# Optimization experiments

Hardware: AMD Instinct MI355X
Metric: run time of the kernel (lower is better)

The kernel has to match this reference:

```python
import jax, jax.numpy as jnp
import numpy as np

SAMPLE_RATE = 16000
SOUND_SPEED = 343.0
MAX_ORDER = 15
RIR_LENGTH = 3968
WINDOW_LENGTH = 81
PAD = WINDOW_LENGTH // 2  # 40

# Static image-source lattice (depends only on max_order): all integer
# reflection index triplets with |nx|+|ny|+|nz| <= max_order.
_ind = np.arange(-MAX_ORDER, MAX_ORDER + 1)
_grid = np.stack(np.meshgrid(_ind, _ind, _ind, indexing="ij"), -1).reshape(-1, 3)
XYZ = _grid[np.abs(_grid).sum(1) <= MAX_ORDER].astype(np.float32)  # (I,3), I=4991
EXP_LO = np.abs(np.floor(XYZ / 2)).astype(np.float32)        # hits on lower walls per dim
EXP_HI = np.abs(np.floor((XYZ + 1) / 2)).astype(np.float32)  # hits on upper walls per dim


def _hann(x, T):
    # continuous Hann window sampled at non-integer points, zero outside |x|<=T/2
    return jnp.where(jnp.abs(x) <= T / 2, 0.5 * (1.0 + jnp.cos(2.0 * jnp.pi * x / T)), 0.0)


def _forward(inp):
    room = inp[:, 0:3]                 # (B,3) room dimensions [m]
    mic = inp[:, 3:6] * room           # (B,3)
    src = inp[:, 6:9] * room           # (B,3)
    a_w = inp[:, 9:10]
    absorption = jnp.concatenate([a_w, a_w, a_w, a_w, inp[:, 10:11], inp[:, 11:12]], axis=1)
    absorption = absorption * 0.84 + 0.01            # (B,6): [x-,x+,y-,y+,floor,ceiling]
    tr = jnp.sqrt(1.0 - absorption)                  # wall reflection coefficients

    xyz = jnp.asarray(XYZ)                           # (I,3)
    d = room[:, None, :]
    s = src[:, None, :]
    # image source locations (B,I,3): mirror parity per torchaudio ISM
    img_loc = jnp.where(xyz % 2 == 1, d * (xyz + 1.0) - s, d * xyz + s)
    # per-image-source attenuation (B,I)
    t_lo = tr[:, None, 0::2]                         # (B,1,3) lower walls per dim
    t_hi = tr[:, None, 1::2]                         # (B,1,3) upper walls per dim
    att = jnp.prod(t_lo ** jnp.asarray(EXP_LO) * t_hi ** jnp.asarray(EXP_HI), axis=-1)

    dist = jnp.linalg.norm(img_loc - mic[:, None, :], axis=-1)   # (B,I)
    amp = att / dist                                              # 1/r spreading
    delay = dist * (SAMPLE_RATE / SOUND_SPEED)                    # fractional sample delay
    delay_i = jnp.ceil(delay)

    # windowed-sinc fractional-delay pulse sampled at n = delay_i-PAD .. delay_i+PAD
    n_rel = jnp.arange(-PAD, PAD + 1, dtype=jnp.float32)          # (W,)
    x = delay_i[..., None] + n_rel - delay[..., None]             # (B,I,W)
    sig = amp[..., None] * jnp.sinc(x) * _hann(x, 2 * PAD)        # (B,I,W)

    # scatter-accumulate pulses at time index n, dropping out-of-range samples
    t_idx = (delay_i[..., None] + n_rel).astype(jnp.int32)        # (B,I,W)
    B = inp.shape[0]
    b_idx = jnp.arange(B, dtype=jnp.int32)[:, None, None]
    rir = jnp.zeros((B, RIR_LENGTH), dtype=sig.dtype).at[b_idx, t_idx].add(sig, mode="drop")

    toa = PAD + SAMPLE_RATE * jnp.linalg.norm(mic - src, axis=1) / SOUND_SPEED  # (B,)
    return rir, toa


def setup_inputs():
    key = jax.random.key(0)
    u = jax.random.uniform(key, (128, 12), dtype=jnp.float32)
    room = 2.0 + 8.0 * u[:, :3]          # room dims in [2,10] m
    rest = 0.05 + 0.9 * u[:, 3:]         # mic/src fractions and absorptions in (0,1)
    return {"input": jnp.concatenate([room, rest], axis=1)}


def reference(input):
    return _forward(input)
```

## Files before the change

kernel.cpp:

```cpp
#include <hip/hip_runtime.h>

#define NIMG    4991
#define RIRLEN  3968
#define NT      512
#define NTP     1024
#define NTG     256
#define NGRPF   16
#define GGRP    32
#define CAP     2048
#define CAPG    1024
#define KPT     10
#define KPTP    5
#define INV_PI  0.31830988618379067f
#define SR_OVER_C 46.647230320699704f

struct Tab { int v[NIMG]; };
static constexpr Tab make_tab() {
    Tab t{};
    int k = 0;
    for (int x = -15; x <= 15; ++x)
        for (int y = -15; y <= 15; ++y)
            for (int z = -15; z <= 15; ++z) {
                int ax = x < 0 ? -x : x;
                int ay = y < 0 ? -y : y;
                int az = z < 0 ? -z : z;
                if (ax + ay + az <= 15)
                    t.v[k++] = (x + 15) | ((y + 15) << 8) | ((z + 15) << 16);
            }
    return t;
}
__constant__ Tab c_tab = make_tab();

static __device__ __forceinline__ int iabs(int v) { return v < 0 ? -v : v; }
static __device__ __forceinline__ int imin(int a, int b) { return a < b ? a : b; }
static __device__ __forceinline__ int imax(int a, int b) { return a > b ? a : b; }

typedef __fp16 f16x2 __attribute__((ext_vector_type(2)));


__global__ __launch_bounds__(NTP)
void rir_prep(const float* __restrict__ inp, float* __restrict__ out,
              float2* __restrict__ wdh, unsigned* __restrict__ wcs,
              int* __restrict__ offs, int B) {
    const int b    = blockIdx.x;
    const int tid  = threadIdx.x;
    const int lane = tid & 63;
    const int wv   = tid >> 6;
    const int q    = lane & 3;

    __shared__ float s_par[12];
    __shared__ float s_p2[3][32];
    __shared__ float s_at[3][32];
    __shared__ int   s_h4[256][4];
    __shared__ int   s_off[257];

    if (tid < 1024) ((int*)s_h4)[tid] = 0;
    if (tid == 0) {
        const float* ip = inp + b * 12;
        float rx = ip[0], ry = ip[1], rz = ip[2];
        float mx = ip[3] * rx, my = ip[4] * ry, mz = ip[5] * rz;
        float sx = ip[6] * rx, sy = ip[7] * ry, sz = ip[8] * rz;
        float aw = __builtin_fmaf(ip[9],  0.84f, 0.01f);
        float a4 = __builtin_fmaf(ip[10], 0.84f, 0.01f);
        float a5 = __builtin_fmaf(ip[11], 0.84f, 0.01f);
        s_par[0] = rx; s_par[1] = ry; s_par[2] = rz;
        s_par[3] = mx; s_par[4] = my; s_par[5] = mz;
        s_par[6] = sx; s_par[7] = sy; s_par[8] = sz;
        s_par[9]  = 0.5f * __builtin_amdgcn_logf(1.0f - aw);
        s_par[10] = 0.5f * __builtin_amdgcn_logf(1.0f - a4);
        s_par[11] = 0.5f * __builtin_amdgcn_logf(1.0f - a5);
        float dx = mx - sx, dy = my - sy, dz = mz - sz;
        out[(size_t)B * RIRLEN + b] = __builtin_fmaf(
            __builtin_sqrtf(dx * dx + dy * dy + dz * dz), SR_OVER_C, 40.0f);
    }
    __syncthreads();

    if (tid < 96) {
        const int axis = tid >> 5;
        const int j    = tid & 31;
        if (j < 31) {
            const int n = j - 15;
            const float rr = s_par[axis];
            const float mm = s_par[3 + axis];
            const float ss = s_par[6 + axis];
            const float iv = (n & 1) ? __builtin_fmaf(rr, (float)(n + 1), -ss)
                                     : __builtin_fmaf(rr, (float)n, ss);
            const float pv = iv - mm;
            s_p2[axis][j] = pv * pv;
            const float e4 = (float)iabs(n >> 1);
            const float e5 = (float)iabs((n + 1) >> 1);
            const float ex = (axis < 2)
                ? (e4 + e5) * s_par[9]
                : __builtin_fmaf(e4, s_par[10], e5 * s_par[11]);
            s_at[axis][j] = __builtin_amdgcn_exp2f(ex);
        }
    }
    __syncthreads();

    float2   edh[KPTP];
    unsigned ecs[KPTP];
    int      enc[KPTP];
    #pragma unroll
    for (int k = 0; k < KPTP; ++k) {
        enc[k] = -1;
        const int idx = tid + k * NTP;
        if (idx < NIMG) {
            const int p  = c_tab.v[idx];
            const int xi = p & 255;
            const int yi = (p >> 8) & 255;
            const int zi = (p >> 16) & 255;
            const float d2   = s_p2[0][xi] + s_p2[1][yi] + s_p2[2][zi];
            const float dist = __builtin_sqrtf(d2);
            const float delay = dist * SR_OVER_C;
            const float di    = __builtin_ceilf(delay);
            const int   ti0   = (int)di - 40;
            if (ti0 < RIRLEN) {
                const int bk = (ti0 + 96) >> 4;
                const float att = s_at[0][xi] * s_at[1][yi] * s_at[2][zi];
                const float amp = att * __builtin_amdgcn_rcpf(dist);
                float frac = di - delay;
                if (frac == 0.0f) frac = di * 1.52587890625e-05f;
                const int dii = (int)di;
                float c1p = amp * __builtin_amdgcn_sinf(0.5f * frac) * INV_PI;
                if (dii & 1) c1p = -c1p;
                const float Hp     = 0.5f * c1p;
                const float dstore = di - frac;
                const float rv = dstore * 0.0125f;
                const float fr = rv - __builtin_floorf(rv);
                const float Hcd = Hp * __builtin_amdgcn_cosf(fr);
                const float Hsd = Hp * __builtin_amdgcn_sinf(fr);
                const f16x2 pk2 = __builtin_amdgcn_cvt_pkrtz(Hcd, Hsd);

                const int rnk = atomicAdd(&s_h4[bk][q], 1);
                enc[k] = (bk << 13) | rnk;
                edh[k] = make_float2(dstore, Hp);
                ecs[k] = __builtin_bit_cast(unsigned, pk2);
            }
        }
    }
    __syncthreads();

    if (wv == 0) {
        const int l = lane;
        const int4 a0 = *(const int4*)&s_h4[4 * l + 0][0];
        const int4 a1 = *(const int4*)&s_h4[4 * l + 1][0];
        const int4 a2 = *(const int4*)&s_h4[4 * l + 2][0];
        const int4 a3 = *(const int4*)&s_h4[4 * l + 3][0];
        const int c0 = a0.x + a0.y + a0.z + a0.w;
        const int c1 = a1.x + a1.y + a1.z + a1.w;
        const int c2 = a2.x + a2.y + a2.z + a2.w;
        const int c3 = a3.x + a3.y + a3.z + a3.w;
        const int ts = c0 + c1 + c2 + c3;
        int incl = ts;
        #pragma unroll
        for (int d = 1; d < 64; d <<= 1) {
            const int u = __shfl_up(incl, d, 64);
            if (l >= d) incl += u;
        }
        const int base = incl - ts;
        s_off[4 * l + 0] = base;
        s_off[4 * l + 1] = base + c0;
        s_off[4 * l + 2] = base + c0 + c1;
        s_off[4 * l + 3] = base + c0 + c1 + c2;
        if (l == 63) s_off[256] = incl;
    }
    __syncthreads();

    if (tid < 256) {
        int run = s_off[tid];
        #pragma unroll
        for (int p = 0; p < 4; ++p) {
            const int c = s_h4[tid][p];
            s_h4[tid][p] = run;
            run += c;
        }
    }
    __syncthreads();

    float2*   db = wdh + (size_t)b * NIMG;
    unsigned* cb = wcs + (size_t)b * NIMG;
    #pragma unroll
    for (int k = 0; k < KPTP; ++k) {
        if (enc[k] >= 0) {
            const int bk   = enc[k] >> 13;
            const int slot = s_h4[bk][q] + (enc[k] & 8191);
            db[slot] = edh[k];
            cb[slot] = ecs[k];
        }
    }
    if (tid < 257) offs[b * 257 + tid] = s_off[tid];
}

__global__ __launch_bounds__(NTG, 8)
void rir_gather(const float2* __restrict__ wdh, const unsigned* __restrict__ wcs,
                const int* __restrict__ offs, float* __restrict__ out, int B) {
    const int bx   = blockIdx.x;
    const int b    = bx >> 5;
    const int g    = bx & 31;
    const int tid  = threadIdx.x;
    const int lane = tid & 63;
    const int wv   = tid >> 6;

    __shared__ __align__(16) float2   s_dh[CAPG];
    __shared__ __align__(16) unsigned s_cs[CAPG];
    __shared__ float s_acc[2][64];

    if (tid < 128) ((float*)s_acc)[tid] = 0.0f;

    const int* ob = offs + b * 257;
    int wlo[2], wlen[2], wpre[2];
    int T = 0, nw = 0;
    #pragma unroll
    for (int kk = 0; kk < 2; ++kk) {
        const int wi = g + 32 * kk;
        wpre[kk] = T;
        if (wi < 62) {
            wlo[kk] = ob[4 * wi + 1];
            int len = ob[4 * wi + 10] - wlo[kk];
            if (T + len > CAPG) len = CAPG - T;
            if (len < 0) len = 0;
            wlen[kk] = len;
            T += len;
            nw = kk + 1;
        } else { wlo[kk] = 0; wlen[kk] = 0; }
    }

    const float2*   db = wdh + (size_t)b * NIMG;
    const unsigned* cb = wcs + (size_t)b * NIMG;
    for (int j = tid; j < T; j += NTG) {
        const int kk  = (j >= wpre[1] && wlen[1] > 0) ? 1 : 0;
        const int src = wlo[kk] + (j - wpre[kk]);
        s_dh[j] = db[src];
        s_cs[j] = cb[src];
    }
    __syncthreads();

    const int a0r = (T * wv) >> 2;
    const int a1r = (T * (wv + 1)) >> 2;

#define EV1(ACC, DLY, HPV, PKU) do {                                         \
        const f16x2 hh = __builtin_bit_cast(f16x2, (PKU));                   \
        const float xw = tf - (DLY);                                         \
        const float pre = __builtin_fmaf(cth0, (float)hh.x,                  \
                              __builtin_fmaf(sth0, (float)hh.y, (HPV)));     \
        const float hm = (__builtin_fabsf(xw) <= 40.0f) ? pre : 0.0f;        \
        ACC = __builtin_fmaf(hm, __builtin_amdgcn_rcpf(xw), ACC);            \
    } while (0)

    #pragma unroll
    for (int kk = 0; kk < 2; ++kk) {
        if (wlen[kk] == 0) continue;
        int       i  = imax(wpre[kk], a0r);
        const int ie = imin(wpre[kk] + wlen[kk], a1r);
        if (i >= ie) continue;

        const int   wi   = g + 32 * kk;
        const int   t    = (wi << 6) + lane;
        const float tf   = (float)t;
        const int   m    = t - (t / 80) * 80;
        const float cth0 = __builtin_amdgcn_cosf((float)m * 0.0125f);
        const float sth0 = __builtin_amdgcn_sinf((float)m * 0.0125f);

        float acc0 = 0.0f, acc1 = 0.0f;
        while (i < ie && (i & 3)) { EV1(acc0, s_dh[i].x, s_dh[i].y, s_cs[i]); ++i; }
        for (; i + 4 <= ie; i += 4) {
            const float4 d0 = *(const float4*)&s_dh[i];
            const float4 d1 = *(const float4*)&s_dh[i + 2];
            const uint4  cc = *(const uint4*)&s_cs[i];
            EV1(acc0, d0.x, d0.y, cc.x); EV1(acc1, d0.z, d0.w, cc.y);
            EV1(acc0, d1.x, d1.y, cc.z); EV1(acc1, d1.z, d1.w, cc.w);
        }
        for (; i < ie; ++i) EV1(acc0, s_dh[i].x, s_dh[i].y, s_cs[i]);

        atomicAdd(&s_acc[kk][lane], acc0 + acc1);
    }
#undef EV1
    __syncthreads();

    if (tid < 64 * nw) {
        const int kk = tid >> 6;
        const int wi = g + 32 * kk;
        const int t  = (wi << 6) + lane;
        const float sl = (lane & 1) ? -1.0f : 1.0f;
        out[(size_t)b * RIRLEN + t] = sl * s_acc[kk][lane];
    }
}

__global__ __launch_bounds__(NT, 8)
void rir_fused(const float* __restrict__ inp, float* __restrict__ out, int B) {
    const int bx   = blockIdx.x;
    const int b    = bx >> 4;
    const int g    = bx & 15;
    const int tid  = threadIdx.x;
    const int lane = tid & 63;
    const int wv   = tid >> 6;
    const int q    = lane & 3;

    __shared__ __align__(16) float2   s_dh[CAP];
    __shared__ __align__(16) unsigned s_cs[CAP];
    __shared__ float    s_par[12];
    __shared__ float    s_p2[3][32];
    __shared__ float    s_at[3][32];
    __shared__ int      s_h4[256][4];
    __shared__ int      s_off[257];
    __shared__ float    s_acc[4][64];

    for (int k = tid; k < 1024; k += NT) ((int*)s_h4)[k] = 0;
    if (tid < 256) ((float*)s_acc)[tid] = 0.0f;
    if (tid == 0) {
        const float* ip = inp + b * 12;
        float rx = ip[0], ry = ip[1], rz = ip[2];
        float mx = ip[3] * rx, my = ip[4] * ry, mz = ip[5] * rz;
        float sx = ip[6] * rx, sy = ip[7] * ry, sz = ip[8] * rz;
        float aw = __builtin_fmaf(ip[9],  0.84f, 0.01f);
        float a4 = __builtin_fmaf(ip[10], 0.84f, 0.01f);
        float a5 = __builtin_fmaf(ip[11], 0.84f, 0.01f);
        s_par[0] = rx; s_par[1] = ry; s_par[2] = rz;
        s_par[3] = mx; s_par[4] = my; s_par[5] = mz;
        s_par[6] = sx; s_par[7] = sy; s_par[8] = sz;
        s_par[9]  = 0.5f * __builtin_amdgcn_logf(1.0f - aw);
        s_par[10] = 0.5f * __builtin_amdgcn_logf(1.0f - a4);
        s_par[11] = 0.5f * __builtin_amdgcn_logf(1.0f - a5);
        if (g == 0) {
            float dx = mx - sx, dy = my - sy, dz = mz - sz;
            out[(size_t)B * RIRLEN + b] = __builtin_fmaf(
                __builtin_sqrtf(dx * dx + dy * dy + dz * dz), SR_OVER_C, 40.0f);
        }
    }
    __syncthreads();

    if (tid < 96) {
        const int axis = tid >> 5;
        const int j    = tid & 31;
        if (j < 31) {
            const int n = j - 15;
            const float rr = s_par[axis];
            const float mm = s_par[3 + axis];
            const float ss = s_par[6 + axis];
            const float iv = (n & 1) ? __builtin_fmaf(rr, (float)(n + 1), -ss)
                                     : __builtin_fmaf(rr, (float)n, ss);
            const float pv = iv - mm;
            s_p2[axis][j] = pv * pv;
            const float e4 = (float)iabs(n >> 1);
            const float e5 = (float)iabs((n + 1) >> 1);
            const float ex = (axis < 2)
                ? (e4 + e5) * s_par[9]
                : __builtin_fmaf(e4, s_par[10], e5 * s_par[11]);
            s_at[axis][j] = __builtin_amdgcn_exp2f(ex);
        }
    }
    __syncthreads();

    const int fb = 4 * g + 1;

    float2   edh[KPT];
    unsigned ecs[KPT];
    int      enc[KPT];
    #pragma unroll
    for (int k = 0; k < KPT; ++k) {
        enc[k] = -1;
        const int idx = tid + k * NT;
        if (idx < NIMG) {
            const int p  = c_tab.v[idx];
            const int xi = p & 255;
            const int yi = (p >> 8) & 255;
            const int zi = (p >> 16) & 255;
            const float d2   = s_p2[0][xi] + s_p2[1][yi] + s_p2[2][zi];
            const float dist = __builtin_sqrtf(d2);
            const float delay = dist * SR_OVER_C;
            const float di    = __builtin_ceilf(delay);
            const int   ti0   = (int)di - 40;
            const int   bk    = (ti0 + 96) >> 4;
            const bool owned  = ((unsigned)((bk - fb + 64) & 63) < 9u);
            if (ti0 < RIRLEN && owned) {
                const float att = s_at[0][xi] * s_at[1][yi] * s_at[2][zi];
                const float amp = att * __builtin_amdgcn_rcpf(dist);
                float frac = di - delay;
                if (frac == 0.0f) frac = di * 1.52587890625e-05f;
                const int dii = (int)di;
                float c1p = amp * __builtin_amdgcn_sinf(0.5f * frac) * INV_PI;
                if (dii & 1) c1p = -c1p;
                const float Hp     = 0.5f * c1p;
                const float dstore = di - frac;
                const float rv = dstore * 0.0125f;
                const float fr = rv - __builtin_floorf(rv);
                const float Hcd = Hp * __builtin_amdgcn_cosf(fr);
                const float Hsd = Hp * __builtin_amdgcn_sinf(fr);
                const f16x2 pk2 = __builtin_amdgcn_cvt_pkrtz(Hcd, Hsd);
                const int rnk = atomicAdd(&s_h4[bk][q], 1);
                enc[k] = (bk << 13) | rnk;
                edh[k] = make_float2(dstore, Hp);
                ecs[k] = __builtin_bit_cast(unsigned, pk2);
            }
        }
    }
    __syncthreads();

    if (wv == 0) {
        const int l = lane;
        const int4 a0 = *(const int4*)&s_h4[4 * l + 0][0];
        const int4 a1 = *(const int4*)&s_h4[4 * l + 1][0];
        const int4 a2 = *(const int4*)&s_h4[4 * l + 2][0];
        const int4 a3 = *(const int4*)&s_h4[4 * l + 3][0];
        const int c0 = a0.x + a0.y + a0.z + a0.w;
        const int c1 = a1.x + a1.y + a1.z + a1.w;
        const int c2 = a2.x + a2.y + a2.z + a2.w;
        const int c3 = a3.x + a3.y + a3.z + a3.w;
        const int ts = c0 + c1 + c2 + c3;
        int incl = ts;
        #pragma unroll
        for (int d = 1; d < 64; d <<= 1) {
            const int u = __shfl_up(incl, d, 64);
            if (l >= d) incl += u;
        }
        const int base = incl - ts;
        s_off[4 * l + 0] = imin(base, CAP);
        s_off[4 * l + 1] = imin(base + c0, CAP);
        s_off[4 * l + 2] = imin(base + c0 + c1, CAP);
        s_off[4 * l + 3] = imin(base + c0 + c1 + c2, CAP);
        if (l == 63) s_off[256] = imin(incl, CAP);
    }
    __syncthreads();

    if (tid < 256) {
        int run = s_off[tid];
        #pragma unroll
        for (int p = 0; p < 4; ++p) {
            const int c = s_h4[tid][p];
            s_h4[tid][p] = run;
            run += c;
        }
    }
    __syncthreads();

    #pragma unroll
    for (int k = 0; k < KPT; ++k) {
        if (enc[k] >= 0) {
            const int bk   = enc[k] >> 13;
            const int slot = s_h4[bk][q] + (enc[k] & 8191);
            if (slot < CAP) {
                s_dh[slot] = edh[k];
                s_cs[slot] = ecs[k];
            }
        }
    }
    __syncthreads();

    int wlo[4], wlen[4], wpre[4];
    int T = 0, nw = 0;
    #pragma unroll
    for (int kk = 0; kk < 4; ++kk) {
        const int wi = g + 16 * kk;
        wpre[kk] = T;
        if (wi < 62) {
            wlo[kk]  = s_off[4 * wi + 1];
            wlen[kk] = s_off[4 * wi + 10] - wlo[kk];
            T += wlen[kk];
            nw = kk + 1;
        } else { wlo[kk] = 0; wlen[kk] = 0; }
    }
    const int a0r = (T * wv) >> 3;
    const int a1r = (T * (wv + 1)) >> 3;

#define EV1(ACC, DLY, HPV, PKU) do {                                         \
        const f16x2 hh = __builtin_bit_cast(f16x2, (PKU));                   \
        const float xw = tf - (DLY);                                         \
        const float pre = __builtin_fmaf(cth0, (float)hh.x,                  \
                              __builtin_fmaf(sth0, (float)hh.y, (HPV)));     \
        const float hm = (__builtin_fabsf(xw) <= 40.0f) ? pre : 0.0f;        \
        ACC = __builtin_fmaf(hm, __builtin_amdgcn_rcpf(xw), ACC);            \
    } while (0)

    #pragma unroll
    for (int kk = 0; kk < 4; ++kk) {
        if (wlen[kk] == 0) continue;
        const int o0 = imax(wpre[kk], a0r);
        const int oe = imin(wpre[kk] + wlen[kk], a1r);
        if (o0 >= oe) continue;
        int       i  = wlo[kk] + (o0 - wpre[kk]);
        const int ie = wlo[kk] + (oe - wpre[kk]);

        const int   wi   = g + 16 * kk;
        const int   t    = (wi << 6) + lane;
        const float tf   = (float)t;
        const int   m    = t - (t / 80) * 80;
        const float cth0 = __builtin_amdgcn_cosf((float)m * 0.0125f);
        const float sth0 = __builtin_amdgcn_sinf((float)m * 0.0125f);

        float acc0 = 0.0f, acc1 = 0.0f;
        while (i < ie && (i & 3)) { EV1(acc0, s_dh[i].x, s_dh[i].y, s_cs[i]); ++i; }
        for (; i + 4 <= ie; i += 4) {
            const float4 d0 = *(const float4*)&s_dh[i];
            const float4 d1 = *(const float4*)&s_dh[i + 2];
            const uint4  cc = *(const uint4*)&s_cs[i];
            EV1(acc0, d0.x, d0.y, cc.x); EV1(acc1, d0.z, d0.w, cc.y);
            EV1(acc0, d1.x, d1.y, cc.z); EV1(acc1, d1.z, d1.w, cc.w);
        }
        for (; i < ie; ++i) EV1(acc0, s_dh[i].x, s_dh[i].y, s_cs[i]);

        atomicAdd(&s_acc[kk][lane], acc0 + acc1);
    }
#undef EV1
    __syncthreads();

    if (tid < 64 * nw) {
        const int kk = tid >> 6;
        const int wi = g + 16 * kk;
        const int t  = (wi << 6) + lane;
        const float sl = (lane & 1) ? -1.0f : 1.0f;
        out[(size_t)b * RIRLEN + t] = sl * s_acc[kk][lane];
    }
}

extern "C" void kernel_launch(void* const* d_in, const int* in_sizes, int n_in,
                              void* d_out, int out_size, void* d_ws, size_t ws_size,
                              hipStream_t stream) {
    (void)n_in; (void)out_size;
    const float* inp = (const float*)d_in[0];
    float* out = (float*)d_out;
    const int B = in_sizes[0] / 12;

    const size_t dh_bytes   = (size_t)B * NIMG * sizeof(float2);
    const size_t cs_bytes   = (size_t)B * NIMG * sizeof(unsigned);
    const size_t offs_bytes = (size_t)B * 257 * sizeof(int);
    const int use_ws = (d_ws != nullptr &&
                        ws_size >= dh_bytes + cs_bytes + offs_bytes) ? 1 : 0;

    if (use_ws) {
        float2*   wdh  = (float2*)d_ws;
        unsigned* wcs  = (unsigned*)((char*)d_ws + dh_bytes);
        int*      offs = (int*)((char*)d_ws + dh_bytes + cs_bytes);
        rir_prep  <<<dim3(B),        dim3(NTP), 0, stream>>>(inp, out, wdh, wcs, offs, B);
        rir_gather<<<dim3(B * GGRP), dim3(NTG), 0, stream>>>(wdh, wcs, offs, out, B);
    } else {
        rir_fused<<<dim3(B * NGRPF), dim3(NT), 0, stream>>>(inp, out, B);
    }
}
```

Before: 104.9 us.

## Pack pulse records as float4 and pair mirrored windows in gather blocks

Prep now writes each image-source record as a single float4 (delay, Hp, Hcd, Hsd) in fp32 instead of a float2 plus a packed fp16 pair. Gather stages one float4 array in LDS and reads it with simpler per-element vector loads. Each gather block now handles windows g and 61-g rather than g and g+32, which balances early dense and late sparse windows across 31 blocks per batch, and the LDS capacity is raised to match. The price is more global and LDS traffic per record and a larger LDS footprint, which may reduce occupancy.

```diff
diff --git a/kernel.cpp b/kernel.cpp
--- a/kernel.cpp
+++ b/kernel.cpp
@@ -6,9 +6,9 @@
 #define NTP     1024
 #define NTG     256
 #define NGRPF   16
-#define GGRP    32
+#define GGRP    31
 #define CAP     2048
-#define CAPG    1024
+#define CAPG    1152
 #define KPT     10
 #define KPTP    5
 #define INV_PI  0.31830988618379067f
@@ -40,8 +40,7 @@
 
 __global__ __launch_bounds__(NTP)
 void rir_prep(const float* __restrict__ inp, float* __restrict__ out,
-              float2* __restrict__ wdh, unsigned* __restrict__ wcs,
-              int* __restrict__ offs, int B) {
+              float4* __restrict__ wq, int* __restrict__ offs, int B) {
     const int b    = blockIdx.x;
     const int tid  = threadIdx.x;
     const int lane = tid & 63;
@@ -97,9 +96,8 @@
     }
     __syncthreads();
 
-    float2   edh[KPTP];
-    unsigned ecs[KPTP];
-    int      enc[KPTP];
+    float4 ef[KPTP];
+    int    enc[KPTP];
     #pragma unroll
     for (int k = 0; k < KPTP; ++k) {
         enc[k] = -1;
@@ -129,12 +127,10 @@
                 const float fr = rv - __builtin_floorf(rv);
                 const float Hcd = Hp * __builtin_amdgcn_cosf(fr);
                 const float Hsd = Hp * __builtin_amdgcn_sinf(fr);
-                const f16x2 pk2 = __builtin_amdgcn_cvt_pkrtz(Hcd, Hsd);
 
                 const int rnk = atomicAdd(&s_h4[bk][q], 1);
                 enc[k] = (bk << 13) | rnk;
-                edh[k] = make_float2(dstore, Hp);
-                ecs[k] = __builtin_bit_cast(unsigned, pk2);
+                ef[k]  = make_float4(dstore, Hp, Hcd, Hsd);
             }
         }
     }
@@ -177,73 +173,64 @@
     }
     __syncthreads();
 
-    float2*   db = wdh + (size_t)b * NIMG;
-    unsigned* cb = wcs + (size_t)b * NIMG;
+    float4* qb = wq + (size_t)b * NIMG;
     #pragma unroll
     for (int k = 0; k < KPTP; ++k) {
         if (enc[k] >= 0) {
             const int bk   = enc[k] >> 13;
             const int slot = s_h4[bk][q] + (enc[k] & 8191);
-            db[slot] = edh[k];
-            cb[slot] = ecs[k];
+            qb[slot] = ef[k];
         }
     }
     if (tid < 257) offs[b * 257 + tid] = s_off[tid];
 }
 
 __global__ __launch_bounds__(NTG, 8)
-void rir_gather(const float2* __restrict__ wdh, const unsigned* __restrict__ wcs,
-                const int* __restrict__ offs, float* __restrict__ out, int B) {
+void rir_gather(const float4* __restrict__ wq, const int* __restrict__ offs,
+                float* __restrict__ out, int B) {
     const int bx   = blockIdx.x;
-    const int b    = bx >> 5;
-    const int g    = bx & 31;
+    const int b    = bx / GGRP;
+    const int g    = bx - b * GGRP;
     const int tid  = threadIdx.x;
     const int lane = tid & 63;
     const int wv   = tid >> 6;
 
-    __shared__ __align__(16) float2   s_dh[CAPG];
-    __shared__ __align__(16) unsigned s_cs[CAPG];
+    __shared__ __align__(16) float4 s_e[CAPG];
     __shared__ float s_acc[2][64];
 
     if (tid < 128) ((float*)s_acc)[tid] = 0.0f;
 
+    const int wis[2] = { g, 61 - g };
     const int* ob = offs + b * 257;
     int wlo[2], wlen[2], wpre[2];
-    int T = 0, nw = 0;
+    int T = 0;
     #pragma unroll
     for (int kk = 0; kk < 2; ++kk) {
-        const int wi = g + 32 * kk;
+        const int wi = wis[kk];
         wpre[kk] = T;
-        if (wi < 62) {
-            wlo[kk] = ob[4 * wi + 1];
-            int len = ob[4 * wi + 10] - wlo[kk];
-            if (T + len > CAPG) len = CAPG - T;
-            if (len < 0) len = 0;
-            wlen[kk] = len;
-            T += len;
-            nw = kk + 1;
-        } else { wlo[kk] = 0; wlen[kk] = 0; }
-    }
-
-    const float2*   db = wdh + (size_t)b * NIMG;
-    const unsigned* cb = wcs + (size_t)b * NIMG;
+        wlo[kk]  = ob[4 * wi + 1];
+        int len  = ob[4 * wi + 10] - wlo[kk];
+        if (T + len > CAPG) len = CAPG - T;
+        if (len < 0) len = 0;
+        wlen[kk] = len;
+        T += len;
+    }
+
+    const float4* qb = wq + (size_t)b * NIMG;
     for (int j = tid; j < T; j += NTG) {
         const int kk  = (j >= wpre[1] && wlen[1] > 0) ? 1 : 0;
-        const int src = wlo[kk] + (j - wpre[kk]);
-        s_dh[j] = db[src];
-        s_cs[j] = cb[src];
+        s_e[j] = qb[wlo[kk] + (j - wpre[kk])];
     }
     __syncthreads();
 
     const int a0r = (T * wv) >> 2;
     const int a1r = (T * (wv + 1)) >> 2;
 
-#define EV1(ACC, DLY, HPV, PKU) do {                                         \
-        const f16x2 hh = __builtin_bit_cast(f16x2, (PKU));                   \
-        const float xw = tf - (DLY);                                         \
-        const float pre = __builtin_fmaf(cth0, (float)hh.x,                  \
-                              __builtin_fmaf(sth0, (float)hh.y, (HPV)));     \
-        const float hm = (__builtin_fabsf(xw) <= 40.0f) ? pre : 0.0f;        \
+#define EV1(ACC, E) do {                                                     \
+        const float xw  = tf - (E).x;                                        \
+        const float pre = __builtin_fmaf(cth0, (E).z,                        \
+                              __builtin_fmaf(sth0, (E).w, (E).y));           \
+        const float hm  = (__builtin_fabsf(xw) <= 40.0f) ? pre : 0.0f;       \
         ACC = __builtin_fmaf(hm, __builtin_amdgcn_rcpf(xw), ACC);            \
     } while (0)
 
@@ -254,7 +241,7 @@
         const int ie = imin(wpre[kk] + wlen[kk], a1r);
         if (i >= ie) continue;
 
-        const int   wi   = g + 32 * kk;
+        const int   wi   = wis[kk];
         const int   t    = (wi << 6) + lane;
         const float tf   = (float)t;
         const int   m    = t - (t / 80) * 80;
@@ -262,24 +249,21 @@
         const float sth0 = __builtin_amdgcn_sinf((float)m * 0.0125f);
 
         float acc0 = 0.0f, acc1 = 0.0f;
-        while (i < ie && (i & 3)) { EV1(acc0, s_dh[i].x, s_dh[i].y, s_cs[i]); ++i; }
         for (; i + 4 <= ie; i += 4) {
-            const float4 d0 = *(const float4*)&s_dh[i];
-            const float4 d1 = *(const float4*)&s_dh[i + 2];
-            const uint4  cc = *(const uint4*)&s_cs[i];
-            EV1(acc0, d0.x, d0.y, cc.x); EV1(acc1, d0.z, d0.w, cc.y);
-            EV1(acc0, d1.x, d1.y, cc.z); EV1(acc1, d1.z, d1.w, cc.w);
-        }
-        for (; i < ie; ++i) EV1(acc0, s_dh[i].x, s_dh[i].y, s_cs[i]);
+            const float4 e0 = s_e[i],     e1 = s_e[i + 1];
+            const float4 e2 = s_e[i + 2], e3 = s_e[i + 3];
+            EV1(acc0, e0); EV1(acc1, e1); EV1(acc0, e2); EV1(acc1, e3);
+        }
+        for (; i < ie; ++i) { const float4 e = s_e[i]; EV1(acc0, e); }
 
         atomicAdd(&s_acc[kk][lane], acc0 + acc1);
     }
 #undef EV1
     __syncthreads();
 
-    if (tid < 64 * nw) {
+    if (tid < 128) {
         const int kk = tid >> 6;
-        const int wi = g + 32 * kk;
+        const int wi = wis[kk];
         const int t  = (wi << 6) + lane;
         const float sl = (lane & 1) ? -1.0f : 1.0f;
         out[(size_t)b * RIRLEN + t] = sl * s_acc[kk][lane];
@@ -520,18 +504,15 @@
     float* out = (float*)d_out;
     const int B = in_sizes[0] / 12;
 
-    const size_t dh_bytes   = (size_t)B * NIMG * sizeof(float2);
-    const size_t cs_bytes   = (size_t)B * NIMG * sizeof(unsigned);
+    const size_t wq_bytes   = (size_t)B * NIMG * sizeof(float4);
     const size_t offs_bytes = (size_t)B * 257 * sizeof(int);
-    const int use_ws = (d_ws != nullptr &&
-                        ws_size >= dh_bytes + cs_bytes + offs_bytes) ? 1 : 0;
+    const int use_ws = (d_ws != nullptr && ws_size >= wq_bytes + offs_bytes) ? 1 : 0;
 
     if (use_ws) {
-        float2*   wdh  = (float2*)d_ws;
-        unsigned* wcs  = (unsigned*)((char*)d_ws + dh_bytes);
-        int*      offs = (int*)((char*)d_ws + dh_bytes + cs_bytes);
-        rir_prep  <<<dim3(B),        dim3(NTP), 0, stream>>>(inp, out, wdh, wcs, offs, B);
-        rir_gather<<<dim3(B * GGRP), dim3(NTG), 0, stream>>>(wdh, wcs, offs, out, B);
+        float4* wq   = (float4*)d_ws;
+        int*    offs = (int*)((char*)d_ws + wq_bytes);
+        rir_prep  <<<dim3(B),        dim3(NTP), 0, stream>>>(inp, out, wq, offs, B);
+        rir_gather<<<dim3(B * GGRP), dim3(NTG), 0, stream>>>(wq, offs, out, B);
     } else {
         rir_fused<<<dim3(B * NGRPF), dim3(NT), 0, stream>>>(inp, out, B);
     }
```

Result: faster. 96.83 us (-7.7%).
